# Kernel tuning notes

Hardware: AMD Instinct MI355X
Metric: run time of the kernel (lower is better)

## Reference

```python
import jax, jax.numpy as jnp
import numpy as np

D = 1024
H = 16
HD = D // H
FF = 2 * D
EPS = 1e-5


def _ln(x, g, b):
    mu = jnp.mean(x, axis=-1, keepdims=True)
    var = jnp.mean(jnp.square(x - mu), axis=-1, keepdims=True)
    return (x - mu) * jax.lax.rsqrt(var + EPS) * g + b


def setup_inputs() -> dict:
    key = jax.random.key(0)
    ks = jax.random.split(key, 16)
    s = 1.0 / np.sqrt(D)
    sf = 1.0 / np.sqrt(FF)
    inp = {
        "x": jax.random.normal(ks[0], (4, 2048, D), dtype=jnp.float32),
        "Wq": jax.random.uniform(ks[1], (D, D), jnp.float32, -s, s),
        "bq": jnp.zeros((D,), jnp.float32),
        "Wk": jax.random.uniform(ks[2], (D, D), jnp.float32, -s, s),
        "bk": jnp.zeros((D,), jnp.float32),
        "Wv": jax.random.uniform(ks[3], (D, D), jnp.float32, -s, s),
        "bv": jnp.zeros((D,), jnp.float32),
        "Wo": jax.random.uniform(ks[4], (D, D), jnp.float32, -s, s),
        "bo": jnp.zeros((D,), jnp.float32),
        "g1": jnp.ones((D,), jnp.float32),
        "b1": jnp.zeros((D,), jnp.float32),
        "g2": jnp.ones((D,), jnp.float32),
        "b2": jnp.zeros((D,), jnp.float32),
        "W1": jax.random.uniform(ks[5], (D, FF), jnp.float32, -s, s),
        "bf1": jnp.zeros((FF,), jnp.float32),
        "W2": jax.random.uniform(ks[6], (FF, D), jnp.float32, -sf, sf),
        "bf2": jnp.zeros((D,), jnp.float32),
    }
    return inp


def reference(x, Wq, bq, Wk, bk, Wv, bv, Wo, bo, g1, b1, g2, b2, W1, bf1, W2, bf2):
    B, S, _ = x.shape
    scale = HD ** -0.5
    residual = x
    xn = _ln(x, g1, b1)
    # QKV projections -> [B, H, S, HD]
    q = (xn @ Wq + bq).reshape(B, S, H, HD).transpose(0, 2, 1, 3)
    k = (xn @ Wk + bk).reshape(B, S, H, HD).transpose(0, 2, 1, 3)
    v = (xn @ Wv + bv).reshape(B, S, H, HD).transpose(0, 2, 1, 3)
    scores = jnp.einsum("bhqd,bhkd->bhqk", q, k) * scale
    attn = jax.nn.softmax(scores, axis=-1)  # dropout is identity at eval
    ctx = jnp.einsum("bhqk,bhkd->bhqd", attn, v)
    ctx = ctx.transpose(0, 2, 1, 3).reshape(B, S, D)
    x = ctx @ Wo + bo + residual
    residual = x
    xn = _ln(x, g2, b2)
    h = jax.nn.gelu(xn @ W1 + bf1, approximate=False)
    return h @ W2 + bf2 + residual
```

## Files before the change

kernel.cpp:

```cpp
#include <hip/hip_runtime.h>
#include <hip/hip_bf16.h>
#include <math.h>

#define D_MODEL 1024
#define H_NUM 16
#define HD 64
#define FF_DIM 2048
#define SEQ 2048
#define BATCH 4
#define M_TOK 8192

typedef __attribute__((ext_vector_type(8))) short bf16x8;
typedef __attribute__((ext_vector_type(4))) float f32x4;
typedef __attribute__((ext_vector_type(16))) float f32x16;
typedef __attribute__((ext_vector_type(4))) unsigned int uint4v;
typedef __attribute__((ext_vector_type(2))) int int2v;

__device__ __forceinline__ short f2bf(float f) {
  __hip_bfloat16 h = __float2bfloat16(f);
  return *reinterpret_cast<short*>(&h);
}

__device__ __forceinline__ void gload16(const void* g, void* l) {
  __builtin_amdgcn_global_load_lds((const __attribute__((address_space(1))) void*)g,
                                   (__attribute__((address_space(3))) void*)l, 16, 0, 0);
}

__device__ __forceinline__ unsigned cvt_pk_bf16(float lo, float hi) {
  unsigned r;
  asm("v_cvt_pk_bf16_f32 %0, %1, %2" : "=v"(r) : "v"(lo), "v"(hi));
  return r;
}

__device__ __forceinline__ float fexp2(float x) {
  float r;
  asm("v_exp_f32 %0, %1" : "=v"(r) : "v"(x));
  return r;
}

__device__ __forceinline__ float frcp(float x) {
  float r;
  asm("v_rcp_f32 %0, %1" : "=v"(r) : "v"(x));
  return r;
}

__device__ __forceinline__ float fmax3(float a, float b, float c) {
  float r;
  asm("v_max3_f32 %0, %1, %2, %3" : "=v"(r) : "v"(a), "v"(b), "v"(c));
  return r;
}

#define BARRIER() __builtin_amdgcn_s_barrier()
#define LGKM0()                                  \
  do {                                           \
    asm volatile("s_waitcnt lgkmcnt(0)");        \
    __builtin_amdgcn_sched_barrier(0);           \
  } while (0)
#define VMC(n)                                   \
  do {                                           \
    asm volatile("s_waitcnt vmcnt(" #n ")");     \
    __builtin_amdgcn_sched_barrier(0);           \
  } while (0)

__global__ __launch_bounds__(256) void transpose_all(
    const float* __restrict__ Wq, const float* __restrict__ Wk,
    const float* __restrict__ Wv, const float* __restrict__ Wo,
    const float* __restrict__ W1, const float* __restrict__ W2,
    short* __restrict__ WqkvT, short* __restrict__ WoT,
    short* __restrict__ W1T, short* __restrict__ W2T) {
  const int bid = blockIdx.x;
  const float* src;
  short* dst;
  int K, N, t;
  if (bid < 256)       { src = Wq; dst = WqkvT;           K = 1024; N = 1024; t = bid; }
  else if (bid < 512)  { src = Wk; dst = WqkvT + 1048576; K = 1024; N = 1024; t = bid - 256; }
  else if (bid < 768)  { src = Wv; dst = WqkvT + 2097152; K = 1024; N = 1024; t = bid - 512; }
  else if (bid < 1024) { src = Wo; dst = WoT;             K = 1024; N = 1024; t = bid - 768; }
  else if (bid < 1536) { src = W1; dst = W1T;             K = 1024; N = 2048; t = bid - 1024; }
  else                 { src = W2; dst = W2T;             K = 2048; N = 1024; t = bid - 1536; }
  const int lg = (N == 2048) ? 5 : 4;
  const int ty = t >> lg, tx = t & ((1 << lg) - 1);
  const int n0 = tx * 64, k0 = ty * 64;

  __shared__ float tile[64][65];
  const int tr = threadIdx.x >> 4;
  const int tc = (threadIdx.x & 15) * 4;
#pragma unroll
  for (int i = 0; i < 4; ++i) {
    int kr = tr + i * 16;
    float4 v = *(const float4*)(src + (size_t)(k0 + kr) * N + n0 + tc);
    tile[kr][tc] = v.x; tile[kr][tc + 1] = v.y; tile[kr][tc + 2] = v.z; tile[kr][tc + 3] = v.w;
  }
  __syncthreads();
#pragma unroll
  for (int i = 0; i < 4; ++i) {
    int r = tr + i * 16;
    short4 o;
    o.x = f2bf(tile[tc][r]);
    o.y = f2bf(tile[tc + 1][r]);
    o.z = f2bf(tile[tc + 2][r]);
    o.w = f2bf(tile[tc + 3][r]);
    *(short4*)(dst + (size_t)(n0 + r) * K + k0 + tc) = o;
  }
}

__global__ __launch_bounds__(256) void transpose_v(const short* __restrict__ src,
                                                   short* __restrict__ dst) {
  __shared__ short t[64][72];
  const int s0 = blockIdx.x * 64;
  const size_t b = (size_t)blockIdx.y * SEQ * HD;
  const int r = threadIdx.x >> 2;
  const int c = (threadIdx.x & 3) * 16;
  *(bf16x8*)&t[r][c] = *(const bf16x8*)(src + b + (size_t)(s0 + r) * HD + c);
  *(bf16x8*)&t[r][c + 8] = *(const bf16x8*)(src + b + (size_t)(s0 + r) * HD + c + 8);
  __syncthreads();
  const int d = threadIdx.x >> 2;
  const int cc = (threadIdx.x & 3) * 16;
  bf16x8 o0, o1;
#pragma unroll
  for (int i = 0; i < 8; ++i) o0[i] = t[cc + i][d];
#pragma unroll
  for (int i = 0; i < 8; ++i) o1[i] = t[cc + 8 + i][d];
  *(bf16x8*)(dst + b + (size_t)d * SEQ + s0 + cc) = o0;
  *(bf16x8*)(dst + b + (size_t)d * SEQ + s0 + cc + 8) = o1;
}

__global__ __launch_bounds__(256) void ln_bf16(const float* __restrict__ x,
                                               const float* __restrict__ g,
                                               const float* __restrict__ b,
                                               short* __restrict__ out) {
  const int row = blockIdx.x;
  const int t = threadIdx.x;
  const float* xr = x + (size_t)row * D_MODEL;
  float4 v = *(const float4*)(xr + t * 4);
  float s = v.x + v.y + v.z + v.w;
  float s2 = v.x * v.x + v.y * v.y + v.z * v.z + v.w * v.w;
#pragma unroll
  for (int m = 1; m < 64; m <<= 1) { s += __shfl_xor(s, m); s2 += __shfl_xor(s2, m); }
  __shared__ float ps[8];
  const int wid = t >> 6, lane = t & 63;
  if (lane == 0) { ps[wid] = s; ps[wid + 4] = s2; }
  __syncthreads();
  s = ps[0] + ps[1] + ps[2] + ps[3];
  s2 = ps[4] + ps[5] + ps[6] + ps[7];
  float mu = s * (1.f / D_MODEL);
  float rstd = rsqrtf(s2 * (1.f / D_MODEL) - mu * mu + 1e-5f);
  float4 gv = *(const float4*)(g + t * 4);
  float4 bv = *(const float4*)(b + t * 4);
  short4 o;
  o.x = f2bf((v.x - mu) * rstd * gv.x + bv.x);
  o.y = f2bf((v.y - mu) * rstd * gv.y + bv.y);
  o.z = f2bf((v.z - mu) * rstd * gv.z + bv.z);
  o.w = f2bf((v.w - mu) * rstd * gv.w + bv.w);
  *(short4*)(out + (size_t)row * D_MODEL + t * 4) = o;
}

template <int BM, int MODE>
__global__ __launch_bounds__(512, 2) void gemm8p(const short* __restrict__ A,
                                                 const short* __restrict__ Bt,
                                                 const float* __restrict__ bias0,
                                                 const float* __restrict__ bias1,
                                                 const float* __restrict__ bias2,
                                                 const float* resid, float* outf,
                                                 short* outb0, short* outb1, short* outb2,
                                                 int M, int N, int K) {
  constexpr int FM = BM / 32;
  constexpr int HM = FM / 2;
  constexpr int GA = BM / 128;
  constexpr int ABUF = BM * 64;
  constexpr int BBUF = 256 * 64;
  constexpr int BUFS = ABUF + BBUF;
  __shared__ short lds[2 * BUFS];

  const int tid = threadIdx.x;
  const int lane = tid & 63;
  const int wid = tid >> 6;
  const int wr = wid >> 2, wc = wid & 3;
  const int l15 = lane & 15, l4 = lane >> 4;

  const int nwg = gridDim.x;
  const int id = blockIdx.x;
  const int swz = (id & 7) * (nwg >> 3) + (id >> 3);
  const int nbx = N >> 8;
  const int by = swz / nbx, bx = swz - by * nbx;
  const int row0 = by * BM, col0 = bx * 256;

  f32x4 acc[FM][4];
#pragma unroll
  for (int i = 0; i < FM; ++i)
#pragma unroll
    for (int j = 0; j < 4; ++j) acc[i][j] = (f32x4){0.f, 0.f, 0.f, 0.f};

  const int NT = K >> 6;

  auto STAGE = [&](int buf, int t, int kh) {
    const int k0 = t * 64 + kh * 32;
    short* ab = lds + buf * BUFS + kh * (BM * 32);
#pragma unroll
    for (int s = 0; s < GA; ++s) {
      const int r = s * 128 + (tid >> 2);
      const int g = (tid & 3) ^ ((r >> 1) & 3);
      gload16(A + (size_t)(row0 + r) * K + k0 + g * 8, ab + s * 4096 + tid * 8);
    }
    short* bb = lds + buf * BUFS + ABUF + kh * (256 * 32);
#pragma unroll
    for (int s = 0; s < 2; ++s) {
      const int r = s * 128 + (tid >> 2);
      const int g = (tid & 3) ^ ((r >> 1) & 3);
      gload16(Bt + (size_t)(col0 + r) * K + k0 + g * 8, bb + s * 4096 + tid * 8);
    }
  };

  auto LDA = [&](bf16x8* dst, int buf, int kh, int h) {
    const short* ab = lds + buf * BUFS + kh * (BM * 32);
#pragma unroll
    for (int i = 0; i < HM; ++i) {
      const int R = wr * (BM / 2) + (h * HM + i) * 16 + l15;
      dst[i] = *(const bf16x8*)(ab + (R >> 1) * 64 + (R & 1) * 32 +
                                ((l4 ^ ((R >> 1) & 3)) << 3));
    }
  };
  auto LDB = [&](bf16x8* dst, int buf, int kh) {
    const short* bb = lds + buf * BUFS + ABUF + kh * (256 * 32);
#pragma unroll
    for (int nf = 0; nf < 4; ++nf) {
      const int R = wc * 64 + nf * 16 + l15;
      dst[nf] = *(const bf16x8*)(bb + (R >> 1) * 64 + (R & 1) * 32 +
                                 ((l4 ^ ((R >> 1) & 3)) << 3));
    }
  };

  bf16x8 Af[HM], Bf[4];

  STAGE(0, 0, 0);
  STAGE(0, 0, 1);
  if (GA == 1) { VMC(3); } else { VMC(4); }
  BARRIER();

  for (int t = 0; t < NT; ++t) {
    const int b = t & 1;
    const bool nst = (t + 1 < NT);

#pragma unroll
    for (int kh = 0; kh < 2; ++kh) {
      LDA(Af, b, kh, 0);
      LDB(Bf, b, kh);
      if (nst) STAGE(b ^ 1, t + 1, kh);
      BARRIER();
      LGKM0();
      __builtin_amdgcn_s_setprio(1);
#pragma unroll
      for (int i = 0; i < HM; ++i)
#pragma unroll
        for (int nf = 0; nf < 4; ++nf)
          acc[i][nf] = __builtin_amdgcn_mfma_f32_16x16x32_bf16(Af[i], Bf[nf], acc[i][nf], 0, 0, 0);
      __builtin_amdgcn_s_setprio(0);
      BARRIER();

      LDA(Af, b, kh, 1);
      BARRIER();
      LGKM0();
      __builtin_amdgcn_s_setprio(1);
#pragma unroll
      for (int i = 0; i < HM; ++i)
#pragma unroll
        for (int nf = 0; nf < 4; ++nf)
          acc[HM + i][nf] =
              __builtin_amdgcn_mfma_f32_16x16x32_bf16(Af[i], Bf[nf], acc[HM + i][nf], 0, 0, 0);
      __builtin_amdgcn_s_setprio(0);
      if (kh == 0) {
        if (nst) {
          if (GA == 1) { VMC(3); } else { VMC(4); }
        } else {
          VMC(0);
        }
      } else {
        if (GA == 1) { VMC(3); } else { VMC(4); }
      }
      BARRIER();
    }
  }

#pragma unroll
  for (int mf = 0; mf < FM; ++mf) {
#pragma unroll
    for (int nf = 0; nf < 4; ++nf) {
      const int rowb = row0 + wr * (BM / 2) + mf * 16 + (l4 << 2);
      const int col = col0 + wc * 64 + nf * 16 + l15;
      if (MODE == 0) {
        const int which = col >> 10, nn = col & 1023;
        const int hh = nn >> 6, dd = nn & 63;
        const float bias = (which == 0 ? bias0[nn] : which == 1 ? bias1[nn] : bias2[nn]);
        short* o = (which == 0 ? outb0 : which == 1 ? outb1 : outb2);
#pragma unroll
        for (int r = 0; r < 4; ++r) {
          const int row = rowb + r;
          float val = acc[mf][nf][r] + bias;
          if (which == 0) val *= 0.18033688011112042f;
          const int bb = row >> 11, s = row & 2047;
          const size_t dst = (((size_t)((bb << 4) + hh) << 11) + s) * HD + dd;
          o[dst] = f2bf(val);
        }
      } else {
#pragma unroll
        for (int r = 0; r < 4; ++r) {
          const int row = rowb + r;
          float val = acc[mf][nf][r];
          if (MODE == 2) {
            val += bias0[col];
            float a = val * val;
            float c1 = fmaf(a, 0.044715f, 1.0f);
            float arg = (val * 2.302116f) * c1;
            arg = fminf(fmaxf(arg, -60.f), 60.f);
            float e = fexp2(arg);
            float gl = val - val * frcp(e + 1.0f);
            outb0[(size_t)row * N + col] = f2bf(gl);
          } else {
            val += bias0[col] + resid[(size_t)row * N + col];
            outf[(size_t)row * N + col] = val;
          }
        }
      }
    }
  }
}

__global__ __launch_bounds__(256) void attn_swp(const short* __restrict__ q,
                                                const short* __restrict__ k,
                                                const short* __restrict__ vT,
                                                short* __restrict__ ctx) {
  __shared__ short Ks[2][4096];
  __shared__ short VTs[2][4096];
  const int tid = threadIdx.x;
  const int lane = tid & 63;
  const int wid = tid >> 6;
  const int hi = lane >> 5, l31 = lane & 31, l7 = lane & 7;
  const int qt = blockIdx.x, bh = blockIdx.y;
  const size_t base = (size_t)bh * SEQ * HD;
  const int q0 = qt * 128 + wid * 32;

  bf16x8 qf[4];
#pragma unroll
  for (int ks = 0; ks < 4; ++ks)
    qf[ks] = *(const bf16x8*)(q + base + (size_t)(q0 + l31) * HD + ks * 16 + hi * 8);

  bf16x8 onesv;
#pragma unroll
  for (int i = 0; i < 8; ++i) onesv[i] = (short)0x3F80;

  f32x16 o0, o1, o2;
#pragma unroll
  for (int r = 0; r < 16; ++r) { o0[r] = 0.f; o1[r] = 0.f; o2[r] = 0.f; }
  float mreg = -1e30f;

  const int sch = (tid & 7) ^ ((tid >> 3) & 7);

#define STAGE_AT(bi, kt)                                                            \
  {                                                                                 \
    const short* kb_ = k + base + (size_t)(kt) * 64 * HD;                           \
    const short* vb_ = vT + base + (size_t)(kt) * 64;                               \
    _Pragma("unroll") for (int p = 0; p < 2; ++p)                                   \
        gload16(kb_ + (size_t)(p * 32 + (tid >> 3)) * HD + sch * 8,                 \
                Ks[bi] + p * 2048 + tid * 8);                                       \
    _Pragma("unroll") for (int p = 0; p < 2; ++p)                                   \
        gload16(vb_ + (size_t)(p * 32 + (tid >> 3)) * SEQ + sch * 8,                \
                VTs[bi] + p * 2048 + tid * 8);                                      \
  }

  STAGE_AT(0, 0);
  __syncthreads();
  int cur = 0;

  for (int kt = 0; kt < SEQ / 64; ++kt) {
    if (kt + 1 < SEQ / 64) STAGE_AT(cur ^ 1, kt + 1);

    f32x16 s0, s1;
#pragma unroll
    for (int r = 0; r < 16; ++r) { s0[r] = 0.f; s1[r] = 0.f; }
#pragma unroll
    for (int ks = 0; ks < 4; ++ks) {
      const int ch = ((ks * 2 + hi) ^ l7) << 3;
      bf16x8 ka0 = *(const bf16x8*)(Ks[cur] + l31 * 64 + ch);
      bf16x8 ka1 = *(const bf16x8*)(Ks[cur] + (32 + l31) * 64 + ch);
      s0 = __builtin_amdgcn_mfma_f32_32x32x16_bf16(ka0, qf[ks], s0, 0, 0, 0);
      s1 = __builtin_amdgcn_mfma_f32_32x32x16_bf16(ka1, qf[ks], s1, 0, 0, 0);
    }

    float pm;
    {
      float t0 = fmax3(s0[0], s0[1], s0[2]);
      float t1 = fmax3(s0[3], s0[4], s0[5]);
      float t2 = fmax3(s0[6], s0[7], s0[8]);
      float t3 = fmax3(s0[9], s0[10], s0[11]);
      float t4 = fmax3(s0[12], s0[13], s0[14]);
      float t5 = fmax3(s0[15], s1[0], s1[1]);
      float t6 = fmax3(s1[2], s1[3], s1[4]);
      float t7 = fmax3(s1[5], s1[6], s1[7]);
      float t8 = fmax3(s1[8], s1[9], s1[10]);
      float t9 = fmax3(s1[11], s1[12], s1[13]);
      float ta = fmaxf(s1[14], s1[15]);
      float u0 = fmax3(t0, t1, t2);
      float u1 = fmax3(t3, t4, t5);
      float u2 = fmax3(t6, t7, t8);
      float u3 = fmaxf(t9, ta);
      pm = fmax3(fmaxf(u0, u1), u2, u3);
    }
    {
      int2v mm = __builtin_amdgcn_permlane32_swap(__builtin_bit_cast(int, pm),
                                                  __builtin_bit_cast(int, pm), false, false);
      pm = fmaxf(__builtin_bit_cast(float, mm[0]), __builtin_bit_cast(float, mm[1]));
    }
    if (!__all(pm <= mreg + 8.f)) {
      float mn = fmaxf(mreg, pm);
      float al = fexp2(mreg - mn);
      mreg = mn;
#pragma unroll
      for (int r = 0; r < 16; ++r) { o0[r] *= al; o1[r] *= al; o2[r] *= al; }
    }

#pragma unroll
    for (int r = 0; r < 16; ++r) s0[r] = fexp2(s0[r] - mreg);
#pragma unroll
    for (int r = 0; r < 16; ++r) s1[r] = fexp2(s1[r] - mreg);

    uint4v pw[4];
#pragma unroll
    for (int t = 0; t < 2; ++t) {
#pragma unroll
      for (int ks = 0; ks < 2; ++ks) {
        const f32x16& st = t ? s1 : s0;
        unsigned x0 = cvt_pk_bf16(st[8 * ks + 0], st[8 * ks + 1]);
        unsigned x1 = cvt_pk_bf16(st[8 * ks + 2], st[8 * ks + 3]);
        unsigned y0 = cvt_pk_bf16(st[8 * ks + 4], st[8 * ks + 5]);
        unsigned y1 = cvt_pk_bf16(st[8 * ks + 6], st[8 * ks + 7]);
        int2v a0 = __builtin_amdgcn_permlane32_swap((int)y0, (int)x0, false, false);
        int2v a1 = __builtin_amdgcn_permlane32_swap((int)y1, (int)x1, false, false);
        pw[t * 2 + ks] = (uint4v){(unsigned)a0[1], (unsigned)a1[1],
                                  (unsigned)a0[0], (unsigned)a1[0]};
      }
    }

#pragma unroll
    for (int s = 0; s < 4; ++s) {
      bf16x8 pf = __builtin_bit_cast(bf16x8, pw[s]);
      const int ch = ((s * 2 + hi) ^ l7) << 3;
      bf16x8 v0 = *(const bf16x8*)(VTs[cur] + l31 * 64 + ch);
      bf16x8 v1 = *(const bf16x8*)(VTs[cur] + (32 + l31) * 64 + ch);
      o0 = __builtin_amdgcn_mfma_f32_32x32x16_bf16(v0, pf, o0, 0, 0, 0);
      o1 = __builtin_amdgcn_mfma_f32_32x32x16_bf16(v1, pf, o1, 0, 0, 0);
      o2 = __builtin_amdgcn_mfma_f32_32x32x16_bf16(onesv, pf, o2, 0, 0, 0);
    }
    __syncthreads();
    cur ^= 1;
  }
#undef STAGE_AT

  const int b = bh >> 4, hh = bh & 15;
  const float inv = 1.f / o2[0];
  const size_t tokoff = ((size_t)(b * SEQ + q0 + l31)) * D_MODEL + hh * HD;
#pragma unroll
  for (int r = 0; r < 16; ++r) {
    const int d = (r & 3) + 8 * (r >> 2) + 4 * hi;
    ctx[tokoff + d] = f2bf(o0[r] * inv);
    ctx[tokoff + 32 + d] = f2bf(o1[r] * inv);
  }
}

extern "C" void kernel_launch(void* const* d_in, const int* in_sizes, int n_in,
                              void* d_out, int out_size, void* d_ws, size_t ws_size,
                              hipStream_t stream) {
  const float* x  = (const float*)d_in[0];
  const float* Wq = (const float*)d_in[1];
  const float* bq = (const float*)d_in[2];
  const float* Wk = (const float*)d_in[3];
  const float* bk = (const float*)d_in[4];
  const float* Wv = (const float*)d_in[5];
  const float* bv = (const float*)d_in[6];
  const float* Wo = (const float*)d_in[7];
  const float* bo = (const float*)d_in[8];
  const float* g1 = (const float*)d_in[9];
  const float* b1 = (const float*)d_in[10];
  const float* g2 = (const float*)d_in[11];
  const float* b2 = (const float*)d_in[12];
  const float* W1 = (const float*)d_in[13];
  const float* bf1 = (const float*)d_in[14];
  const float* W2 = (const float*)d_in[15];
  const float* bf2 = (const float*)d_in[16];

  char* w = (char*)d_ws;
  short* WqkvT = (short*)w; w += (size_t)3072 * 1024 * 2;
  short* WoT   = (short*)w; w += (size_t)1024 * 1024 * 2;
  short* W1T   = (short*)w; w += (size_t)2048 * 1024 * 2;
  short* W2T   = (short*)w; w += (size_t)1024 * 2048 * 2;
  short* xn    = (short*)w; w += (size_t)M_TOK * 1024 * 2;
  short* qb    = (short*)w; w += (size_t)M_TOK * 1024 * 2;
  short* kb    = (short*)w; w += (size_t)M_TOK * 1024 * 2;
  short* vTb   = (short*)w; w += (size_t)M_TOK * 1024 * 2;
  short* ctxb  = (short*)w; w += (size_t)M_TOK * 1024 * 2;
  short* xn2   = (short*)w; w += (size_t)M_TOK * 1024 * 2;
  short* hb    = (short*)w; w += (size_t)M_TOK * 2048 * 2;
  short* vb    = hb;

  dim3 blk(256);

  transpose_all<<<dim3(2048), blk, 0, stream>>>(Wq, Wk, Wv, Wo, W1, W2,
                                                WqkvT, WoT, W1T, W2T);

  ln_bf16<<<M_TOK, blk, 0, stream>>>(x, g1, b1, xn);

  gemm8p<128, 0><<<dim3(12 * 64), dim3(512), 0, stream>>>(
      xn, WqkvT, bq, bk, bv, nullptr, nullptr, qb, kb, vb, M_TOK, 3072, 1024);

  transpose_v<<<dim3(SEQ / 64, BATCH * H_NUM), blk, 0, stream>>>(vb, vTb);

  attn_swp<<<dim3(16, 64), blk, 0, stream>>>(qb, kb, vTb, ctxb);

  gemm8p<128, 1><<<dim3(4 * 64), dim3(512), 0, stream>>>(
      ctxb, WoT, bo, nullptr, nullptr, x, (float*)d_out, nullptr, nullptr, nullptr,
      M_TOK, 1024, 1024);

  ln_bf16<<<M_TOK, blk, 0, stream>>>((const float*)d_out, g2, b2, xn2);

  gemm8p<256, 2><<<dim3(8 * 32), dim3(512), 0, stream>>>(
      xn2, W1T, bf1, nullptr, nullptr, nullptr, nullptr, hb, nullptr, nullptr,
      M_TOK, 2048, 1024);

  gemm8p<128, 3><<<dim3(4 * 64), dim3(512), 0, stream>>>(
      hb, W2T, bf2, nullptr, nullptr, (const float*)d_out, (float*)d_out,
      nullptr, nullptr, nullptr, M_TOK, 1024, 2048);
}
```

Baseline: 321.9 us.

## Replace double-buffered GEMM pipeline with 4-slot LDS ring, prefetch depth three

The GEMM main loop now streams 32-wide K slices through a four-slot LDS ring. It prefetches three slices ahead and uses a single barrier per slice, replacing the two-buffer scheme that needed several barriers and split A-fragment loads per step. All row fragments are loaded at once, so MFMAs issue in one batch, at the cost of more fragment registers. The QKV projection also moves to a 256-row tile with half as many workgroups. Total LDS footprint per block is unchanged.

```diff
diff --git a/kernel.cpp b/kernel.cpp
--- a/kernel.cpp
+++ b/kernel.cpp
@@ -156,21 +156,20 @@
 }
 
 template <int BM, int MODE>
-__global__ __launch_bounds__(512, 2) void gemm8p(const short* __restrict__ A,
-                                                 const short* __restrict__ Bt,
-                                                 const float* __restrict__ bias0,
-                                                 const float* __restrict__ bias1,
-                                                 const float* __restrict__ bias2,
-                                                 const float* resid, float* outf,
-                                                 short* outb0, short* outb1, short* outb2,
-                                                 int M, int N, int K) {
+__global__ __launch_bounds__(512, 2) void gemm_ring(const short* __restrict__ A,
+                                                    const short* __restrict__ Bt,
+                                                    const float* __restrict__ bias0,
+                                                    const float* __restrict__ bias1,
+                                                    const float* __restrict__ bias2,
+                                                    const float* resid, float* outf,
+                                                    short* outb0, short* outb1, short* outb2,
+                                                    int M, int N, int K) {
   constexpr int FM = BM / 32;
-  constexpr int HM = FM / 2;
   constexpr int GA = BM / 128;
-  constexpr int ABUF = BM * 64;
-  constexpr int BBUF = 256 * 64;
-  constexpr int BUFS = ABUF + BBUF;
-  __shared__ short lds[2 * BUFS];
+  constexpr int ASLOT = BM * 32;
+  constexpr int BSLOT = 256 * 32;
+  constexpr int SLOT = ASLOT + BSLOT;
+  __shared__ short lds[4 * SLOT];
 
   const int tid = threadIdx.x;
   const int lane = tid & 63;
@@ -191,18 +190,18 @@
 #pragma unroll
     for (int j = 0; j < 4; ++j) acc[i][j] = (f32x4){0.f, 0.f, 0.f, 0.f};
 
-  const int NT = K >> 6;
-
-  auto STAGE = [&](int buf, int t, int kh) {
-    const int k0 = t * 64 + kh * 32;
-    short* ab = lds + buf * BUFS + kh * (BM * 32);
+  const int NH = K >> 5;
+
+  auto STAGE = [&](int h) {
+    const int k0 = h * 32;
+    short* ab = lds + (h & 3) * SLOT;
 #pragma unroll
     for (int s = 0; s < GA; ++s) {
       const int r = s * 128 + (tid >> 2);
       const int g = (tid & 3) ^ ((r >> 1) & 3);
       gload16(A + (size_t)(row0 + r) * K + k0 + g * 8, ab + s * 4096 + tid * 8);
     }
-    short* bb = lds + buf * BUFS + ABUF + kh * (256 * 32);
+    short* bb = ab + ASLOT;
 #pragma unroll
     for (int s = 0; s < 2; ++s) {
       const int r = s * 128 + (tid >> 2);
@@ -211,74 +210,46 @@
     }
   };
 
-  auto LDA = [&](bf16x8* dst, int buf, int kh, int h) {
-    const short* ab = lds + buf * BUFS + kh * (BM * 32);
-#pragma unroll
-    for (int i = 0; i < HM; ++i) {
-      const int R = wr * (BM / 2) + (h * HM + i) * 16 + l15;
-      dst[i] = *(const bf16x8*)(ab + (R >> 1) * 64 + (R & 1) * 32 +
-                                ((l4 ^ ((R >> 1) & 3)) << 3));
-    }
-  };
-  auto LDB = [&](bf16x8* dst, int buf, int kh) {
-    const short* bb = lds + buf * BUFS + ABUF + kh * (256 * 32);
-#pragma unroll
-    for (int nf = 0; nf < 4; ++nf) {
-      const int R = wc * 64 + nf * 16 + l15;
-      dst[nf] = *(const bf16x8*)(bb + (R >> 1) * 64 + (R & 1) * 32 +
+  bf16x8 Af[FM], Bf[4];
+
+  STAGE(0);
+  STAGE(1);
+  STAGE(2);
+
+  for (int h = 0; h < NH; ++h) {
+    if (h + 2 < NH) {
+      if constexpr (GA == 1) { VMC(6); } else { VMC(8); }
+    } else if (h + 1 < NH) {
+      if constexpr (GA == 1) { VMC(3); } else { VMC(4); }
+    } else {
+      VMC(0);
+    }
+    BARRIER();
+    {
+      const short* ab = lds + (h & 3) * SLOT;
+#pragma unroll
+      for (int i = 0; i < FM; ++i) {
+        const int R = wr * (BM / 2) + i * 16 + l15;
+        Af[i] = *(const bf16x8*)(ab + (R >> 1) * 64 + (R & 1) * 32 +
                                  ((l4 ^ ((R >> 1) & 3)) << 3));
-    }
-  };
-
-  bf16x8 Af[HM], Bf[4];
-
-  STAGE(0, 0, 0);
-  STAGE(0, 0, 1);
-  if (GA == 1) { VMC(3); } else { VMC(4); }
-  BARRIER();
-
-  for (int t = 0; t < NT; ++t) {
-    const int b = t & 1;
-    const bool nst = (t + 1 < NT);
-
-#pragma unroll
-    for (int kh = 0; kh < 2; ++kh) {
-      LDA(Af, b, kh, 0);
-      LDB(Bf, b, kh);
-      if (nst) STAGE(b ^ 1, t + 1, kh);
-      BARRIER();
-      LGKM0();
-      __builtin_amdgcn_s_setprio(1);
-#pragma unroll
-      for (int i = 0; i < HM; ++i)
-#pragma unroll
-        for (int nf = 0; nf < 4; ++nf)
-          acc[i][nf] = __builtin_amdgcn_mfma_f32_16x16x32_bf16(Af[i], Bf[nf], acc[i][nf], 0, 0, 0);
-      __builtin_amdgcn_s_setprio(0);
-      BARRIER();
-
-      LDA(Af, b, kh, 1);
-      BARRIER();
-      LGKM0();
-      __builtin_amdgcn_s_setprio(1);
-#pragma unroll
-      for (int i = 0; i < HM; ++i)
-#pragma unroll
-        for (int nf = 0; nf < 4; ++nf)
-          acc[HM + i][nf] =
-              __builtin_amdgcn_mfma_f32_16x16x32_bf16(Af[i], Bf[nf], acc[HM + i][nf], 0, 0, 0);
-      __builtin_amdgcn_s_setprio(0);
-      if (kh == 0) {
-        if (nst) {
-          if (GA == 1) { VMC(3); } else { VMC(4); }
-        } else {
-          VMC(0);
-        }
-      } else {
-        if (GA == 1) { VMC(3); } else { VMC(4); }
       }
-      BARRIER();
-    }
+      const short* bb = ab + ASLOT;
+#pragma unroll
+      for (int nf = 0; nf < 4; ++nf) {
+        const int R = wc * 64 + nf * 16 + l15;
+        Bf[nf] = *(const bf16x8*)(bb + (R >> 1) * 64 + (R & 1) * 32 +
+                                  ((l4 ^ ((R >> 1) & 3)) << 3));
+      }
+    }
+    if (h + 3 < NH) STAGE(h + 3);
+    LGKM0();
+    __builtin_amdgcn_s_setprio(1);
+#pragma unroll
+    for (int i = 0; i < FM; ++i)
+#pragma unroll
+      for (int nf = 0; nf < 4; ++nf)
+        acc[i][nf] = __builtin_amdgcn_mfma_f32_16x16x32_bf16(Af[i], Bf[nf], acc[i][nf], 0, 0, 0);
+    __builtin_amdgcn_s_setprio(0);
   }
 
 #pragma unroll
@@ -508,24 +479,24 @@
 
   ln_bf16<<<M_TOK, blk, 0, stream>>>(x, g1, b1, xn);
 
-  gemm8p<128, 0><<<dim3(12 * 64), dim3(512), 0, stream>>>(
+  gemm_ring<256, 0><<<dim3(12 * 32), dim3(512), 0, stream>>>(
       xn, WqkvT, bq, bk, bv, nullptr, nullptr, qb, kb, vb, M_TOK, 3072, 1024);
 
   transpose_v<<<dim3(SEQ / 64, BATCH * H_NUM), blk, 0, stream>>>(vb, vTb);
 
   attn_swp<<<dim3(16, 64), blk, 0, stream>>>(qb, kb, vTb, ctxb);
 
-  gemm8p<128, 1><<<dim3(4 * 64), dim3(512), 0, stream>>>(
+  gemm_ring<128, 1><<<dim3(4 * 64), dim3(512), 0, stream>>>(
       ctxb, WoT, bo, nullptr, nullptr, x, (float*)d_out, nullptr, nullptr, nullptr,
       M_TOK, 1024, 1024);
 
   ln_bf16<<<M_TOK, blk, 0, stream>>>((const float*)d_out, g2, b2, xn2);
 
-  gemm8p<256, 2><<<dim3(8 * 32), dim3(512), 0, stream>>>(
+  gemm_ring<256, 2><<<dim3(8 * 32), dim3(512), 0, stream>>>(
       xn2, W1T, bf1, nullptr, nullptr, nullptr, nullptr, hb, nullptr, nullptr,
       M_TOK, 2048, 1024);
 
-  gemm8p<128, 3><<<dim3(4 * 64), dim3(512), 0, stream>>>(
+  gemm_ring<128, 3><<<dim3(4 * 64), dim3(512), 0, stream>>>(
       hb, W2T, bf2, nullptr, nullptr, (const float*)d_out, (float*)d_out,
       nullptr, nullptr, nullptr, M_TOK, 1024, 2048);
 }
```

After: 317.1 us. Within noise of the previous version (-1.5%).
